# Optimization experiments

Measured on AMD Instinct MI355X. Metric: run time of the kernel, lower is better.

The kernel has to match this reference:

```python
import jax, jax.numpy as jnp
import numpy as np

B, S, D, H = 2, 1024, 1024, 2048
E = 8          # hash_size: number of expert FFNs
DICT = 32000   # dict_size: vocab for the hash map


def setup_inputs() -> dict:
    key = jax.random.key(0)
    k = jax.random.split(key, 7)
    x = jax.random.normal(k[0], (B, S, D), dtype=jnp.float32)
    orig_input = jax.random.randint(k[1], (B, S), 0, DICT, dtype=jnp.int32)
    # random token -> expert hash map (random.randrange(0, hashsize) in original)
    hash_map = jax.random.randint(k[2], (DICT,), 0, E, dtype=jnp.int32)
    # torch Linear weights are [out, in]; xavier_uniform for weights, default uniform for biases
    lim1 = float(np.sqrt(6.0 / (D + H)))
    lim2 = float(np.sqrt(6.0 / (H + D)))
    W1 = jax.random.uniform(k[3], (E, H, D), minval=-lim1, maxval=lim1, dtype=jnp.float32)
    b1 = jax.random.uniform(k[4], (E, H), minval=-1.0 / np.sqrt(D), maxval=1.0 / np.sqrt(D), dtype=jnp.float32)
    W2 = jax.random.uniform(k[5], (E, D, H), minval=-lim2, maxval=lim2, dtype=jnp.float32)
    b2 = jax.random.uniform(k[6], (E, D), minval=-1.0 / np.sqrt(H), maxval=1.0 / np.sqrt(H), dtype=jnp.float32)
    return {"x": x, "orig_input": orig_input, "hash_map": hash_map,
            "W1": W1, "b1": b1, "W2": W2, "b2": b2}


def reference(x, orig_input, hash_map, W1, b1, W2, b2):
    # expert id per token (hash routing)
    e = hash_map[orig_input]                      # [B, S]
    out = jnp.zeros_like(x)
    # loop over the small fixed set of experts; each iteration is a dense
    # 2-layer FFN, with the token->expert mask selecting which outputs land.
    # (relu_dropout = 0 -> identity; eval-mode semantics)
    for i in range(E):
        h = jax.nn.relu(jnp.einsum('bsd,hd->bsh', x, W1[i]) + b1[i])   # [B,S,H]
        y = jnp.einsum('bsh,dh->bsd', h, W2[i]) + b2[i]                # [B,S,D]
        out = jnp.where((e == i)[..., None], y, out)
    return out
```

## Files before the change

### kernel.cpp

```cpp
#include <hip/hip_runtime.h>
#include <hip/hip_bf16.h>
#include <stdint.h>

#define TOKENS 2048
#define DD 1024
#define HH 2048
#define NE 8
#define RP_CAP 3072
#define BM 128
#define BN 128
#define BK 64

typedef float f32x4 __attribute__((ext_vector_type(4)));
typedef short bf16x8 __attribute__((ext_vector_type(8)));
typedef unsigned int u32;

__device__ __forceinline__ unsigned short f2bf(float f) {
    union { float f; u32 u; } v; v.f = f;
    u32 u = v.u;
    return (unsigned short)((u + 0x7fffu + ((u >> 16) & 1u)) >> 16);
}

__global__ __launch_bounds__(256) void k_route(const int* __restrict__ orig,
                                               const int* __restrict__ hmap,
                                               int* __restrict__ hdr) {
    __shared__ int s_e[TOKENS];
    __shared__ int s_cnt[NE];
    __shared__ int s_off[NE];
    int tid = threadIdx.x;
    if (tid < NE) s_cnt[tid] = 0;
    __syncthreads();
    for (int t = tid; t < TOKENS; t += 256) {
        int e = hmap[orig[t]];
        s_e[t] = e;
        atomicAdd(&s_cnt[e], 1);
    }
    __syncthreads();
    if (tid == 0) {
        int run = 0;
        for (int e = 0; e < NE; ++e) {
            s_off[e] = run;
            hdr[e] = s_cnt[e];
            hdr[8 + e] = run;
            run += ((s_cnt[e] + BM - 1) / BM) * BM;
        }
        hdr[16] = run;
    }
    __syncthreads();
    int* perm = hdr + 64;
    for (int r = tid; r < RP_CAP; r += 256) perm[r] = -1;
    if (tid < NE) s_cnt[tid] = 0;
    __syncthreads();
    for (int t = tid; t < TOKENS; t += 256) {
        int e = s_e[t];
        int pos = s_off[e] + atomicAdd(&s_cnt[e], 1);
        perm[pos] = t;
    }
}

__global__ __launch_bounds__(256) void k_gather(const float* __restrict__ x,
                                                const int* __restrict__ hdr,
                                                unsigned short* __restrict__ xp) {
    int r = blockIdx.x;
    int t = hdr[64 + r];
    int tid = threadIdx.x;
    ushort4* dst = (ushort4*)(xp + (size_t)r * DD);
    if (t >= 0) {
        const float4* src = (const float4*)(x + (size_t)t * DD);
        float4 v = src[tid];
        ushort4 o;
        o.x = f2bf(v.x); o.y = f2bf(v.y); o.z = f2bf(v.z); o.w = f2bf(v.w);
        dst[tid] = o;
    } else {
        ushort4 z; z.x = 0; z.y = 0; z.z = 0; z.w = 0;
        dst[tid] = z;
    }
}

template<int KDIM, int NDIM, bool L2EPI>
__global__ __launch_bounds__(512, 2) void k_gemm(const unsigned short* __restrict__ A,
                                                 const float* __restrict__ W,
                                                 const float* __restrict__ bias,
                                                 const int* __restrict__ hdr,
                                                 unsigned short* __restrict__ hout,
                                                 float* __restrict__ out) {
    int total = hdr[16];
    int row0 = blockIdx.y * BM;
    if (row0 >= total) return;
    int e = 0;
#pragma unroll
    for (int i = 1; i < NE; ++i)
        if (row0 >= hdr[8 + i]) e = i;

    int n0 = blockIdx.x * BN;
    const float* We = W + (size_t)e * NDIM * KDIM;
    const float* be = bias + (size_t)e * NDIM;

    __shared__ __align__(16) unsigned short As[2 * BM * BK];
    __shared__ __align__(16) unsigned short Bs[2 * BN * BK];

    int tid = threadIdx.x;
    int w = tid >> 6, lane = tid & 63;
    int wr = w >> 2, wc = w & 3;
    int fr = lane & 15, hi = lane >> 4;

    f32x4 acc[4][2];
#pragma unroll
    for (int m = 0; m < 4; ++m)
#pragma unroll
        for (int n = 0; n < 2; ++n) acc[m][n] = f32x4{0.f, 0.f, 0.f, 0.f};

    float4 bv[4];

    auto STAGE_A = [&](int buf, int k0) {
#pragma unroll
        for (int j = 0; j < 2; ++j) {
            int c = j * 512 + tid;
            int row = c >> 3;
            int slot = c & 7;
            int gslot = slot ^ (row & 7);
            const unsigned short* gp = A + (size_t)(row0 + row) * KDIM + k0 + gslot * 8;
            unsigned short* lp = (unsigned short*)As + buf * (BM * BK) + (j * 8 + w) * 512;
            __builtin_amdgcn_global_load_lds((const __attribute__((address_space(1))) u32*)gp,
                                             (__attribute__((address_space(3))) u32*)lp, 16, 0, 0);
        }
    };
    auto B_LOAD = [&](int k0) {
#pragma unroll
        for (int jr = 0; jr < 2; ++jr) {
            int c = jr * 512 + tid;
            int row = c >> 3;
            int cl = c & 7;
            const float4* gp = (const float4*)(We + (size_t)(n0 + row) * KDIM + k0 + cl * 8);
            bv[jr * 2]     = gp[0];
            bv[jr * 2 + 1] = gp[1];
        }
    };
    auto B_WRITE = [&](int buf) {
        unsigned short* Bb = Bs + buf * (BN * BK);
#pragma unroll
        for (int jr = 0; jr < 2; ++jr) {
            int c = jr * 512 + tid;
            int row = c >> 3;
            int cl = c & 7;
            float4 v0 = bv[jr * 2], v1 = bv[jr * 2 + 1];
            union { bf16x8 v; unsigned short s[8]; } o;
            o.s[0] = f2bf(v0.x); o.s[1] = f2bf(v0.y); o.s[2] = f2bf(v0.z); o.s[3] = f2bf(v0.w);
            o.s[4] = f2bf(v1.x); o.s[5] = f2bf(v1.y); o.s[6] = f2bf(v1.z); o.s[7] = f2bf(v1.w);
            int sp = cl ^ (row & 7);
            *(bf16x8*)&Bb[row * 64 + sp * 8] = o.v;
        }
    };

    constexpr int NT = KDIM / BK;

    STAGE_A(0, 0);
    B_LOAD(0);
    B_WRITE(0);
    __syncthreads();

    for (int t = 0; t < NT; ++t) {
        int cur = t & 1;
        bool pf = (t + 1 < NT);
        if (pf) {
            STAGE_A(cur ^ 1, (t + 1) * BK);
            B_LOAD((t + 1) * BK);
        }
        const unsigned short* Ab = As + cur * (BM * BK);
        const unsigned short* Bb = Bs + cur * (BN * BK);
#pragma unroll
        for (int kk = 0; kk < BK; kk += 32) {
            bf16x8 af[4], bfr[2];
#pragma unroll
            for (int m = 0; m < 4; ++m) {
                int rr = wr * 64 + m * 16 + fr;
                int idx = (rr * 64 + kk + hi * 8) ^ ((rr & 7) << 3);
                af[m] = *(const bf16x8*)&Ab[idx];
            }
#pragma unroll
            for (int n = 0; n < 2; ++n) {
                int cn = wc * 32 + n * 16 + fr;
                int idx = (cn * 64 + kk + hi * 8) ^ ((cn & 7) << 3);
                bfr[n] = *(const bf16x8*)&Bb[idx];
            }
#pragma unroll
            for (int m = 0; m < 4; ++m)
#pragma unroll
                for (int n = 0; n < 2; ++n)
                    acc[m][n] = __builtin_amdgcn_mfma_f32_16x16x32_bf16(af[m], bfr[n], acc[m][n], 0, 0, 0);
        }
        if (pf) B_WRITE(cur ^ 1);
        __syncthreads();
    }

    const int* perm = hdr + 64;
    int rbase = row0 + wr * 64 + hi * 4;
    int cbase = n0 + wc * 32 + fr;
    if constexpr (!L2EPI) {
#pragma unroll
        for (int n = 0; n < 2; ++n) {
            int cg = cbase + n * 16;
            float bvv = be[cg];
#pragma unroll
            for (int m = 0; m < 4; ++m) {
                int rg = rbase + m * 16;
#pragma unroll
                for (int r = 0; r < 4; ++r) {
                    float v = acc[m][n][r] + bvv;
                    v = v > 0.f ? v : 0.f;
                    hout[(size_t)(rg + r) * NDIM + cg] = f2bf(v);
                }
            }
        }
    } else {
        float bvv[2];
#pragma unroll
        for (int n = 0; n < 2; ++n) bvv[n] = be[cbase + n * 16];
#pragma unroll
        for (int m = 0; m < 4; ++m) {
            int rg = rbase + m * 16;
#pragma unroll
            for (int r = 0; r < 4; ++r) {
                int t = perm[rg + r];
                if (t < 0) continue;
                float* op = out + (size_t)t * DD;
#pragma unroll
                for (int n = 0; n < 2; ++n)
                    op[cbase + n * 16] = acc[m][n][r] + bvv[n];
            }
        }
    }
}

extern "C" void kernel_launch(void* const* d_in, const int* in_sizes, int n_in,
                              void* d_out, int out_size, void* d_ws, size_t ws_size,
                              hipStream_t stream) {
    const float* x    = (const float*)d_in[0];
    const int*   orig = (const int*)d_in[1];
    const int*   hmap = (const int*)d_in[2];
    const float* W1   = (const float*)d_in[3];
    const float* b1   = (const float*)d_in[4];
    const float* W2   = (const float*)d_in[5];
    const float* b2   = (const float*)d_in[6];
    float* out = (float*)d_out;

    int* hdr = (int*)d_ws;
    unsigned short* xp   = (unsigned short*)((char*)d_ws + 16384);
    unsigned short* hbuf = (unsigned short*)((char*)d_ws + 16384 + (size_t)RP_CAP * DD * 2);

    k_route<<<1, 256, 0, stream>>>(orig, hmap, hdr);
    k_gather<<<RP_CAP, 256, 0, stream>>>(x, hdr, xp);
    k_gemm<DD, HH, false><<<dim3(HH / BN, RP_CAP / BM), 512, 0, stream>>>(xp, W1, b1, hdr, hbuf, nullptr);
    k_gemm<HH, DD, true><<<dim3(DD / BN, RP_CAP / BM), 512, 0, stream>>>(hbuf, W2, b2, hdr, nullptr, out);
}
```

Baseline: 88.26 us.

## Prefetch weight tiles two steps ahead with register double-buffering and manual waitcnt

The GEMM main loop is unrolled by two and keeps two register sets for fp32 weight tiles, so global loads of W are issued two K-steps ahead. Explicit s_waitcnt vmcnt(4) and raw barriers replace __syncthreads, letting the in-flight next weight load stay outstanding across the barrier. The aim is to hide global memory latency for the fp32 weight stream. In exchange it raises register pressure, and it relies on the hand-counted vmcnt being correct for both the LDS-direct A loads and the B loads.

New measurement: 86.62 us. No clear change (-1.9%).

```diff
diff --git a/kernel.cpp b/kernel.cpp
--- a/kernel.cpp
+++ b/kernel.cpp
@@ -110,7 +110,7 @@
 #pragma unroll
         for (int n = 0; n < 2; ++n) acc[m][n] = f32x4{0.f, 0.f, 0.f, 0.f};
 
-    float4 bv[4];
+    float4 bvA[4], bvB[4];
 
     auto STAGE_A = [&](int buf, int k0) {
 #pragma unroll
@@ -125,7 +125,7 @@
                                              (__attribute__((address_space(3))) u32*)lp, 16, 0, 0);
         }
     };
-    auto B_LOAD = [&](int k0) {
+    auto B_LOAD = [&](float4 (&bv)[4], int k0) {
 #pragma unroll
         for (int jr = 0; jr < 2; ++jr) {
             int c = jr * 512 + tid;
@@ -136,7 +136,7 @@
             bv[jr * 2 + 1] = gp[1];
         }
     };
-    auto B_WRITE = [&](int buf) {
+    auto B_WRITE = [&](const float4 (&bv)[4], int buf) {
         unsigned short* Bb = Bs + buf * (BN * BK);
 #pragma unroll
         for (int jr = 0; jr < 2; ++jr) {
@@ -151,23 +151,9 @@
             *(bf16x8*)&Bb[row * 64 + sp * 8] = o.v;
         }
     };
-
-    constexpr int NT = KDIM / BK;
-
-    STAGE_A(0, 0);
-    B_LOAD(0);
-    B_WRITE(0);
-    __syncthreads();
-
-    for (int t = 0; t < NT; ++t) {
-        int cur = t & 1;
-        bool pf = (t + 1 < NT);
-        if (pf) {
-            STAGE_A(cur ^ 1, (t + 1) * BK);
-            B_LOAD((t + 1) * BK);
-        }
-        const unsigned short* Ab = As + cur * (BM * BK);
-        const unsigned short* Bb = Bs + cur * (BN * BK);
+    auto COMPUTE = [&](int buf) {
+        const unsigned short* Ab = As + buf * (BM * BK);
+        const unsigned short* Bb = Bs + buf * (BN * BK);
 #pragma unroll
         for (int kk = 0; kk < BK; kk += 32) {
             bf16x8 af[4], bfr[2];
@@ -189,9 +175,42 @@
                 for (int n = 0; n < 2; ++n)
                     acc[m][n] = __builtin_amdgcn_mfma_f32_16x16x32_bf16(af[m], bfr[n], acc[m][n], 0, 0, 0);
         }
-        if (pf) B_WRITE(cur ^ 1);
-        __syncthreads();
-    }
+    };
+
+    constexpr int NT = KDIM / BK;
+
+#define WAIT_KEEP4 asm volatile("s_waitcnt vmcnt(4) lgkmcnt(0)" ::: "memory")
+#define WAIT_ALL   asm volatile("s_waitcnt vmcnt(0) lgkmcnt(0)" ::: "memory")
+#define BARRIER    do { __builtin_amdgcn_s_barrier(); asm volatile("" ::: "memory"); } while (0)
+
+    STAGE_A(0, 0);
+    B_LOAD(bvA, 0);
+    B_LOAD(bvB, BK);
+    B_WRITE(bvA, 0);
+    WAIT_KEEP4;
+    BARRIER;
+
+    for (int t = 0; t < NT; t += 2) {
+        STAGE_A(1, (t + 1) * BK);
+        if (t + 2 < NT) B_LOAD(bvA, (t + 2) * BK);
+        COMPUTE(0);
+        B_WRITE(bvB, 1);
+        if (t + 2 < NT) WAIT_KEEP4; else WAIT_ALL;
+        BARRIER;
+        if (t + 2 < NT) {
+            STAGE_A(0, (t + 2) * BK);
+            if (t + 3 < NT) B_LOAD(bvB, (t + 3) * BK);
+            COMPUTE(1);
+            B_WRITE(bvA, 0);
+            if (t + 3 < NT) WAIT_KEEP4; else WAIT_ALL;
+            BARRIER;
+        } else {
+            COMPUTE(1);
+        }
+    }
+#undef WAIT_KEEP4
+#undef WAIT_ALL
+#undef BARRIER
 
     const int* perm = hdr + 64;
     int rbase = row0 + wr * 64 + hi * 4;
```
